# Optimization experiments

Measured on AMD Instinct MI355X. Metric: run time of the kernel, lower is better.

## Reference

```python
import jax, jax.numpy as jnp
import numpy as np

S, R, CM, CZ, H = 128, 256, 256, 128, 8
HD = CM // H
INF = 1e9
EPS = 1e-5


def _ln(x, g, b):
    mu = jnp.mean(x, axis=-1, keepdims=True)
    var = jnp.var(x, axis=-1, keepdims=True)
    return (x - mu) * jax.lax.rsqrt(var + EPS) * g + b


def setup_inputs() -> dict:
    key = jax.random.key(0)
    ks = jax.random.split(key, 12)
    d = {
        'm': jax.random.normal(ks[0], (S, R, CM), jnp.float32),
        'z': jax.random.normal(ks[1], (R, R, CZ), jnp.float32),
        'mask': jnp.ones((S, R), jnp.float32),
        'ln_m_g': jnp.ones((CM,), jnp.float32),
        'ln_m_b': jnp.zeros((CM,), jnp.float32),
        'ln_z_g': jnp.ones((CZ,), jnp.float32),
        'ln_z_b': jnp.zeros((CZ,), jnp.float32),
        'w_z': jax.random.normal(ks[2], (CZ, H), jnp.float32) * 0.02,
        'wq': jax.random.normal(ks[3], (CM, CM), jnp.float32) * (1.0 / np.sqrt(CM)),
        'wk': jax.random.normal(ks[4], (CM, CM), jnp.float32) * (1.0 / np.sqrt(CM)),
        'wv': jax.random.normal(ks[5], (CM, CM), jnp.float32) * (1.0 / np.sqrt(CM)),
        'wg': jnp.zeros((CM, CM), jnp.float32),
        'bg': jnp.ones((CM,), jnp.float32),
        'wo': jax.random.normal(ks[6], (CM, CM), jnp.float32) * (1.0 / np.sqrt(CM)),
        'bo': jnp.zeros((CM,), jnp.float32),
    }
    return d


def reference(m, z, mask, ln_m_g, ln_m_b, ln_z_g, ln_z_b, w_z, wq, wk, wv, wg, bg, wo, bo):
    # pair bias: LN(z) -> per-head bias [H, R, R], broadcast over seq rows
    z_ln = _ln(z, ln_z_g, ln_z_b)
    pair_bias = jnp.einsum('ijc,ch->hij', z_ln, w_z)          # [H, R, R]
    mask_bias = (INF * (mask - 1.0))[:, None, None, :]        # [S, 1, 1, R]

    m_ln = _ln(m, ln_m_g, ln_m_b)                             # [S, R, CM]
    q = (m_ln @ wq).reshape(S, R, H, HD)
    k = (m_ln @ wk).reshape(S, R, H, HD)
    v = (m_ln @ wv).reshape(S, R, H, HD)

    scale = 1.0 / np.sqrt(HD).astype(np.float32)
    logits = jnp.einsum('sihd,sjhd->shij', q * scale, k)       # [S, H, R, R]
    logits = logits + pair_bias[None] + mask_bias
    attn = jax.nn.softmax(logits, axis=-1)

    o = jnp.einsum('shij,sjhd->sihd', attn, v).reshape(S, R, CM)
    g = jax.nn.sigmoid(m_ln @ wg + bg)
    return (g * o) @ wo + bo
```

## Files before the change

### kernel.cpp

```cpp
#include <hip/hip_runtime.h>
#include <hip/hip_bf16.h>

typedef unsigned short u16;
typedef __bf16 bf16x8 __attribute__((ext_vector_type(8)));
typedef float f32x4 __attribute__((ext_vector_type(4)));
typedef float f32x16 __attribute__((ext_vector_type(16)));
typedef unsigned short u16x8 __attribute__((ext_vector_type(8)));
typedef unsigned short u16x4 __attribute__((ext_vector_type(4)));


__device__ __forceinline__ u16 f2bf(float f) {
  union { float f; unsigned u; } v; v.f = f;
  unsigned r = v.u;
  r += 0x7fffu + ((r >> 16) & 1u);
  return (u16)(r >> 16);
}
__device__ __forceinline__ float bf2f(u16 u) {
  union { unsigned u; float f; } v; v.u = ((unsigned)u) << 16;
  return v.f;
}

__global__ __launch_bounds__(256) void k_prep_w(
    const float* __restrict__ wq, const float* __restrict__ wk,
    const float* __restrict__ wv, const float* __restrict__ wg,
    const float* __restrict__ wo, u16* __restrict__ dst) {
  const int widx = blockIdx.x >> 4;
  const int tid = blockIdx.x & 15;
  const int ri = (tid >> 2) * 64;
  const int ci = (tid & 3) * 64;
  const float* src = (widx == 0) ? wq : (widx == 1) ? wk : (widx == 2) ? wv
                    : (widx == 3) ? wg : wo;
  __shared__ float lt[64][68];
  const int t = threadIdx.x;
  {
    const int r = t >> 2;
    #pragma unroll
    for (int i = 0; i < 4; ++i) {
      const int c = (t & 3) * 16 + i * 4;
      *(float4*)&lt[r][c] = *(const float4*)&src[(ri + r) * 256 + ci + c];
    }
  }
  __syncthreads();
  #pragma unroll
  for (int cc = 0; cc < 2; ++cc) {
    const int c = t + cc * 256;
    const int kb = c >> 8, cb = (c >> 6) & 3, lg = (c >> 4) & 3, lr = c & 15;
    u16x8 o;
    #pragma unroll
    for (int j = 0; j < 8; ++j) o[j] = f2bf(lt[kb * 32 + lg * 8 + j][cb * 16 + lr]);
    const size_t idx = (size_t)widx * 65536 + (size_t)((ci >> 4) + cb) * 4096
                     + (size_t)((ri >> 5) + kb) * 512 + (size_t)(lg * 16 + lr) * 8;
    *(u16x8*)&dst[idx] = o;
  }
}

__global__ __launch_bounds__(256) void k_pair_bias(
    const float* __restrict__ z, const float* __restrict__ zg,
    const float* __restrict__ zb, const float* __restrict__ wz,
    float* __restrict__ pbp) {
  const int t = threadIdx.x;
  const int lane = t & 63, wave = t >> 6;
  const int ql = lane & 15;
  const int p = blockIdx.x * 16 + wave * 4 + (lane >> 4);
  const float4 zv0 = *(const float4*)(z + (size_t)p * 128 + ql * 8);
  const float4 zv1 = *(const float4*)(z + (size_t)p * 128 + ql * 8 + 4);
  float s = zv0.x + zv0.y + zv0.z + zv0.w + zv1.x + zv1.y + zv1.z + zv1.w;
  float sq = zv0.x * zv0.x + zv0.y * zv0.y + zv0.z * zv0.z + zv0.w * zv0.w
           + zv1.x * zv1.x + zv1.y * zv1.y + zv1.z * zv1.z + zv1.w * zv1.w;
  #pragma unroll
  for (int o = 8; o > 0; o >>= 1) { s += __shfl_xor(s, o); sq += __shfl_xor(sq, o); }
  const float mu = s * 0.0078125f;
  const float var = sq * 0.0078125f - mu * mu;
  const float rs = rsqrtf(var + 1e-5f);
  const int c0 = ql * 8;
  float zn[8];
  zn[0] = (zv0.x - mu) * rs * zg[c0 + 0] + zb[c0 + 0];
  zn[1] = (zv0.y - mu) * rs * zg[c0 + 1] + zb[c0 + 1];
  zn[2] = (zv0.z - mu) * rs * zg[c0 + 2] + zb[c0 + 2];
  zn[3] = (zv0.w - mu) * rs * zg[c0 + 3] + zb[c0 + 3];
  zn[4] = (zv1.x - mu) * rs * zg[c0 + 4] + zb[c0 + 4];
  zn[5] = (zv1.y - mu) * rs * zg[c0 + 5] + zb[c0 + 5];
  zn[6] = (zv1.z - mu) * rs * zg[c0 + 6] + zb[c0 + 6];
  zn[7] = (zv1.w - mu) * rs * zg[c0 + 7] + zb[c0 + 7];
  float a[8] = {};
  #pragma unroll
  for (int i = 0; i < 8; ++i) {
    #pragma unroll
    for (int hh = 0; hh < 8; ++hh) a[hh] += zn[i] * wz[(c0 + i) * 8 + hh];
  }
  #pragma unroll
  for (int hh = 0; hh < 8; ++hh) {
    #pragma unroll
    for (int o = 8; o > 0; o >>= 1) a[hh] += __shfl_xor(a[hh], o);
  }
  if (ql == 0) {
    const int i = p >> 8, j = p & 255;
    const int strip = i >> 5, il = i & 31, jt = j >> 5, r = j & 31;
    const int gh = (r >> 2) & 1, qd = r >> 3, c4 = r & 3;
    const int off = (strip * 8 + jt) * 1024 + (gh * 32 + il) * 16 + qd * 4 + c4;
    #pragma unroll
    for (int hh = 0; hh < 8; ++hh) pbp[(size_t)hh * 65536 + off] = a[hh];
  }
}

__global__ __launch_bounds__(256) void k_ln_m(
    const float* __restrict__ m, const float* __restrict__ gam,
    const float* __restrict__ bet, u16* __restrict__ mln) {
  const int lane = threadIdx.x & 63;
  const size_t row = (size_t)blockIdx.x * 4 + (threadIdx.x >> 6);
  const float4 xv = *(const float4*)(m + row * 256 + lane * 4);
  float s = xv.x + xv.y + xv.z + xv.w;
  float sq = xv.x * xv.x + xv.y * xv.y + xv.z * xv.z + xv.w * xv.w;
  #pragma unroll
  for (int o = 32; o > 0; o >>= 1) { s += __shfl_xor(s, o); sq += __shfl_xor(sq, o); }
  const float mu = s * 0.00390625f;
  const float var = sq * 0.00390625f - mu * mu;
  const float rs = rsqrtf(var + 1e-5f);
  const int c = lane * 4;
  u16x4 o4;
  o4.x = f2bf((xv.x - mu) * rs * gam[c] + bet[c]);
  o4.y = f2bf((xv.y - mu) * rs * gam[c + 1] + bet[c + 1]);
  o4.z = f2bf((xv.z - mu) * rs * gam[c + 2] + bet[c + 2]);
  o4.w = f2bf((xv.w - mu) * rs * gam[c + 3] + bet[c + 3]);
  *(u16x4*)(mln + row * 256 + c) = o4;
}

__global__ __launch_bounds__(256, 2) void k_fused(
    const u16* __restrict__ mln, const u16* __restrict__ wtp,
    const float* __restrict__ bg, const float* __restrict__ pbp,
    const float* __restrict__ mask, u16* __restrict__ g,
    u16* __restrict__ go) {
  __shared__ u16 lA[32 * 256];
  __shared__ u16 lQ[256 * 32];
  __shared__ u16 lK[256 * 32];
  __shared__ u16 lVt[32][276];
  __shared__ float lMb[256];
  __shared__ float lL[4][32];
  const int bid = blockIdx.x;
  const int s = bid & 127, h = bid >> 7;
  const int t = threadIdx.x;
  const int lane = t & 63, wave = t >> 6;
  const int il = lane & 31, gh = lane >> 5;

  const u16* Wb = wtp + (size_t)wave * 65536 + (size_t)(2 * h + (il >> 4)) * 4096
                + gh * 128 + (il & 15) * 8;
  bf16x8 B[16];
  #pragma unroll
  for (int kc = 0; kc < 16; ++kc) B[kc] = *(const bf16x8*)&Wb[kc * 256];
  __builtin_amdgcn_sched_barrier(0);

  lMb[t] = 1e9f * (mask[s * 256 + t] - 1.0f);
  const float bgv = bg[h * 32 + il];
  const size_t mbase = (size_t)s * 65536;

  #pragma unroll 1
  for (int c = 0; c < 8; ++c) {
    #pragma unroll
    for (int i = 0; i < 4; ++i) {
      const int r = i * 8 + (t >> 5);
      const int cc = (t & 31) * 8;
      *(u16x8*)((char*)lA + ((r * 512 + cc * 2) ^ ((r & 7) << 4))) =
          *(const u16x8*)&mln[mbase + (size_t)(c * 32 + r) * 256 + cc];
    }
    __syncthreads();
    f32x16 acc = {};
    #pragma unroll
    for (int kc = 0; kc < 16; ++kc) {
      const bf16x8 af = *(const bf16x8*)((const char*)lA +
          ((il * 512 + (kc * 16 + gh * 8) * 2) ^ ((il & 7) << 4)));
      acc = __builtin_amdgcn_mfma_f32_32x32x16_bf16(af, B[kc], acc, 0, 0, 0);
    }
    if (wave == 0) {
      #pragma unroll
      for (int reg = 0; reg < 16; ++reg) {
        const int R = c * 32 + (reg & 3) + 8 * (reg >> 2) + 4 * gh;
        *(u16*)((char*)lQ + ((R * 64 + il * 2) ^ ((R & 7) << 4))) =
            f2bf(acc[reg] * 0.17677669529663687f);
      }
    } else if (wave == 1) {
      #pragma unroll
      for (int reg = 0; reg < 16; ++reg) {
        const int R = c * 32 + (reg & 3) + 8 * (reg >> 2) + 4 * gh;
        *(u16*)((char*)lK + ((R * 64 + il * 2) ^ ((R & 7) << 4))) = f2bf(acc[reg]);
      }
    } else if (wave == 2) {
      #pragma unroll
      for (int reg = 0; reg < 16; ++reg) {
        const int R = c * 32 + (reg & 3) + 8 * (reg >> 2) + 4 * gh;
        lVt[il][R] = f2bf(acc[reg]);
      }
    } else {
      #pragma unroll
      for (int reg = 0; reg < 16; ++reg) {
        const int R = c * 32 + (reg & 3) + 8 * (reg >> 2) + 4 * gh;
        const float x = acc[reg] + bgv;
        g[(size_t)(s * 256 + R) * 256 + h * 32 + il] =
            f2bf(1.0f / (1.0f + __expf(-x)));
      }
    }
    __syncthreads();
  }

  #pragma unroll 1
  for (int strip = 0; strip < 2; ++strip) {
    const int i0 = wave * 64 + strip * 32;
    bf16x8 qf[2];
    #pragma unroll
    for (int kk = 0; kk < 2; ++kk) {
      const int row = i0 + il;
      qf[kk] = *(const bf16x8*)((const char*)lQ +
          ((row * 64 + (kk * 16 + gh * 8) * 2) ^ ((row & 7) << 4)));
    }
    const float* pbt = pbp + ((size_t)h * 8 + (i0 >> 5)) * 8192 + lane * 16;

    f32x16 oacc0 = {}, oacc1 = {};
    float s0 = 0.f, s1 = 0.f, s2 = 0.f, s3 = 0.f;

    #pragma unroll 2
    for (int jt = 0; jt < 8; ++jt) {
      const float* pl = pbt + jt * 1024;
      f32x16 c;
      #pragma unroll
      for (int qd = 0; qd < 4; ++qd) {
        const f32x4 pbq = *(const f32x4*)&pl[qd * 4];
        const int jb = jt * 32 + qd * 8 + gh * 4;
        #pragma unroll
        for (int c4 = 0; c4 < 4; ++c4)
          c[qd * 4 + c4] = pbq[c4] + lMb[jb + c4] - 16.0f;
      }
      const int krow = jt * 32 + il;
      const bf16x8 kf0 = *(const bf16x8*)((const char*)lK +
          ((krow * 64 + (gh * 8) * 2) ^ ((krow & 7) << 4)));
      const bf16x8 kf1 = *(const bf16x8*)((const char*)lK +
          ((krow * 64 + (16 + gh * 8) * 2) ^ ((krow & 7) << 4)));
      c = __builtin_amdgcn_mfma_f32_32x32x16_bf16(kf0, qf[0], c, 0, 0, 0);
      c = __builtin_amdgcn_mfma_f32_32x32x16_bf16(kf1, qf[1], c, 0, 0, 0);
      union PK { __bf16 h[4]; uint2 u; } pk[4];
      #pragma unroll
      for (int qd = 0; qd < 4; ++qd) {
        const float p0 = __expf(c[qd * 4 + 0]);
        const float p1 = __expf(c[qd * 4 + 1]);
        const float p2 = __expf(c[qd * 4 + 2]);
        const float p3 = __expf(c[qd * 4 + 3]);
        s0 += p0; s1 += p1; s2 += p2; s3 += p3;
        pk[qd].h[0] = (__bf16)p0; pk[qd].h[1] = (__bf16)p1;
        pk[qd].h[2] = (__bf16)p2; pk[qd].h[3] = (__bf16)p3;
      }
      const uint2 sA = gh ? pk[0].u : pk[1].u;
      uint2 rA; rA.x = __shfl_xor(sA.x, 32); rA.y = __shfl_xor(sA.y, 32);
      const uint2 sB = gh ? pk[2].u : pk[3].u;
      uint2 rB; rB.x = __shfl_xor(sB.x, 32); rB.y = __shfl_xor(sB.y, 32);
      union FR { uint2 u2[2]; bf16x8 v; } fa0, fa1;
      fa0.u2[0] = gh ? rA : pk[0].u;
      fa0.u2[1] = gh ? pk[1].u : rA;
      fa1.u2[0] = gh ? rB : pk[2].u;
      fa1.u2[1] = gh ? pk[3].u : rB;
      const bf16x8 vf0 = *(const bf16x8*)&lVt[il][jt * 32 + gh * 8];
      const bf16x8 vf1 = *(const bf16x8*)&lVt[il][jt * 32 + 16 + gh * 8];
      oacc0 = __builtin_amdgcn_mfma_f32_32x32x16_bf16(fa0.v, vf0, oacc0, 0, 0, 0);
      oacc1 = __builtin_amdgcn_mfma_f32_32x32x16_bf16(fa1.v, vf1, oacc1, 0, 0, 0);
    }

    float lsum = (s0 + s1) + (s2 + s3);
    lsum += __shfl_xor(lsum, 32);
    if (lane < 32) lL[wave][il] = 1.0f / lsum;

    #pragma unroll
    for (int qd = 0; qd < 4; ++qd) {
      const f32x4 invq = *(const f32x4*)&lL[wave][qd * 8 + gh * 4];
      #pragma unroll
      for (int c4 = 0; c4 < 4; ++c4) {
        const int iloc = qd * 8 + gh * 4 + c4;
        const size_t row = (size_t)s * 256 + i0 + iloc;
        const int col = h * 32 + il;
        const float ov = (oacc0[qd * 4 + c4] + oacc1[qd * 4 + c4]) * invq[c4];
        go[row * 256 + col] = f2bf(bf2f(g[row * 256 + col]) * ov);
      }
    }
  }
}

__global__ __launch_bounds__(256, 4) void k_gemm_out(
    const u16* __restrict__ go, const u16* __restrict__ wop,
    const float* __restrict__ bo, float* __restrict__ out) {
  __shared__ u16 lA[32 * 256];
  const int t = threadIdx.x;
  const size_t row0 = (size_t)blockIdx.x * 32;
  const int lane = t & 63, wave = t >> 6;
  const u16* Wz = wop + (size_t)wave * 16384 + (size_t)lane * 8;
  u16x8 areg[4];
  #pragma unroll
  for (int i = 0; i < 4; ++i)
    areg[i] = *(const u16x8*)&go[(row0 + i * 8 + (t >> 5)) * 256 + (t & 31) * 8];
  bf16x8 B[4][4];
  #pragma unroll
  for (int kc = 0; kc < 4; ++kc) {
    #pragma unroll
    for (int nn = 0; nn < 4; ++nn)
      B[kc][nn] = *(const bf16x8*)&Wz[nn * 4096 + kc * 512];
  }
  __builtin_amdgcn_sched_barrier(0);
  #pragma unroll
  for (int i = 0; i < 4; ++i) {
    const int r = i * 8 + (t >> 5);
    const int c = (t & 31) * 8;
    *(u16x8*)((char*)lA + ((r * 512 + c * 2) ^ ((r & 7) << 4))) = areg[i];
  }
  __syncthreads();
  const int lrow = lane & 15, lg = lane >> 4;
  f32x4 acc[2][4] = {};
  #pragma unroll
  for (int kc = 0; kc < 4; ++kc) {
    bf16x8 af[2];
    #pragma unroll
    for (int mm = 0; mm < 2; ++mm) {
      const int row = mm * 16 + lrow;
      af[mm] = *(const bf16x8*)((const char*)lA +
          ((row * 512 + kc * 64 + lg * 16) ^ ((row & 7) << 4)));
    }
    #pragma unroll
    for (int mm = 0; mm < 2; ++mm) {
      #pragma unroll
      for (int nn = 0; nn < 4; ++nn)
        acc[mm][nn] = __builtin_amdgcn_mfma_f32_16x16x32_bf16(
            af[mm], B[kc][nn], acc[mm][nn], 0, 0, 0);
    }
  }
  #pragma unroll
  for (int kc = 0; kc < 4; ++kc) {
    #pragma unroll
    for (int nn = 0; nn < 4; ++nn)
      B[kc][nn] = *(const bf16x8*)&Wz[nn * 4096 + (kc + 4) * 512];
  }
  __builtin_amdgcn_sched_barrier(0);
  #pragma unroll
  for (int kc = 0; kc < 4; ++kc) {
    bf16x8 af[2];
    #pragma unroll
    for (int mm = 0; mm < 2; ++mm) {
      const int row = mm * 16 + lrow;
      af[mm] = *(const bf16x8*)((const char*)lA +
          ((row * 512 + (kc + 4) * 64 + lg * 16) ^ ((row & 7) << 4)));
    }
    #pragma unroll
    for (int mm = 0; mm < 2; ++mm) {
      #pragma unroll
      for (int nn = 0; nn < 4; ++nn)
        acc[mm][nn] = __builtin_amdgcn_mfma_f32_16x16x32_bf16(
            af[mm], B[kc][nn], acc[mm][nn], 0, 0, 0);
    }
  }
  const int wc = wave * 64, lg4 = lg * 4;
  #pragma unroll
  for (int mm = 0; mm < 2; ++mm) {
    #pragma unroll
    for (int nn = 0; nn < 4; ++nn) {
      const int col = wc + nn * 16 + lrow;
      #pragma unroll
      for (int jr = 0; jr < 4; ++jr) {
        const size_t row = row0 + mm * 16 + lg4 + jr;
        out[row * 256 + col] = acc[mm][nn][jr] + bo[col];
      }
    }
  }
}

extern "C" void kernel_launch(void* const* d_in, const int* in_sizes, int n_in,
                              void* d_out, int out_size, void* d_ws, size_t ws_size,
                              hipStream_t stream) {
  const float* m      = (const float*)d_in[0];
  const float* z      = (const float*)d_in[1];
  const float* mask   = (const float*)d_in[2];
  const float* ln_m_g = (const float*)d_in[3];
  const float* ln_m_b = (const float*)d_in[4];
  const float* ln_z_g = (const float*)d_in[5];
  const float* ln_z_b = (const float*)d_in[6];
  const float* w_z    = (const float*)d_in[7];
  const float* wq     = (const float*)d_in[8];
  const float* wk     = (const float*)d_in[9];
  const float* wv     = (const float*)d_in[10];
  const float* wg     = (const float*)d_in[11];
  const float* bg     = (const float*)d_in[12];
  const float* wo     = (const float*)d_in[13];
  const float* bo     = (const float*)d_in[14];
  float* out = (float*)d_out;

  char* w = (char*)d_ws;
  u16* wtp   = (u16*)w;   w += (size_t)5 * 65536 * 2;
  float* pbp = (float*)w; w += (size_t)8 * 65536 * 4;
  u16* mln   = (u16*)w;   w += (size_t)32768 * 256 * 2;
  u16* gow   = (u16*)w;   w += (size_t)32768 * 256 * 2;
  u16* gw    = (u16*)w;   w += (size_t)32768 * 256 * 2;

  k_prep_w   <<<80, 256, 0, stream>>>(wq, wk, wv, wg, wo, wtp);
  k_pair_bias<<<4096, 256, 0, stream>>>(z, ln_z_g, ln_z_b, w_z, pbp);
  k_ln_m     <<<8192, 256, 0, stream>>>(m, ln_m_g, ln_m_b, mln);
  k_fused    <<<1024, 256, 0, stream>>>(mln, wtp, bg, pbp, mask, gw, gow);
  k_gemm_out <<<1024, 256, 0, stream>>>(gow, wtp + (size_t)4 * 65536, bo, out);
}
```

Before: 122.9 us.

## Merge prep kernels, keep gate on-chip, prefetch A tiles, use exp2 softmax

```diff
diff --git a/kernel.cpp b/kernel.cpp
--- a/kernel.cpp
+++ b/kernel.cpp
@@ -8,128 +8,123 @@
 typedef unsigned short u16x8 __attribute__((ext_vector_type(8)));
 typedef unsigned short u16x4 __attribute__((ext_vector_type(4)));
 
-
-__device__ __forceinline__ u16 f2bf(float f) {
-  union { float f; unsigned u; } v; v.f = f;
-  unsigned r = v.u;
-  r += 0x7fffu + ((r >> 16) & 1u);
-  return (u16)(r >> 16);
+#define LOG2E 1.4426950408889634f
+
+__device__ __forceinline__ u16 f2b(float f) {
+  union { __bf16 b; u16 u; } v; v.b = (__bf16)f; return v.u;
 }
 __device__ __forceinline__ float bf2f(u16 u) {
   union { unsigned u; float f; } v; v.u = ((unsigned)u) << 16;
   return v.f;
 }
 
-__global__ __launch_bounds__(256) void k_prep_w(
+__global__ __launch_bounds__(256) void k_pre(
     const float* __restrict__ wq, const float* __restrict__ wk,
     const float* __restrict__ wv, const float* __restrict__ wg,
-    const float* __restrict__ wo, u16* __restrict__ dst) {
-  const int widx = blockIdx.x >> 4;
-  const int tid = blockIdx.x & 15;
-  const int ri = (tid >> 2) * 64;
-  const int ci = (tid & 3) * 64;
-  const float* src = (widx == 0) ? wq : (widx == 1) ? wk : (widx == 2) ? wv
-                    : (widx == 3) ? wg : wo;
-  __shared__ float lt[64][68];
-  const int t = threadIdx.x;
-  {
-    const int r = t >> 2;
-    #pragma unroll
-    for (int i = 0; i < 4; ++i) {
-      const int c = (t & 3) * 16 + i * 4;
-      *(float4*)&lt[r][c] = *(const float4*)&src[(ri + r) * 256 + ci + c];
-    }
-  }
-  __syncthreads();
-  #pragma unroll
-  for (int cc = 0; cc < 2; ++cc) {
-    const int c = t + cc * 256;
-    const int kb = c >> 8, cb = (c >> 6) & 3, lg = (c >> 4) & 3, lr = c & 15;
-    u16x8 o;
-    #pragma unroll
-    for (int j = 0; j < 8; ++j) o[j] = f2bf(lt[kb * 32 + lg * 8 + j][cb * 16 + lr]);
-    const size_t idx = (size_t)widx * 65536 + (size_t)((ci >> 4) + cb) * 4096
-                     + (size_t)((ri >> 5) + kb) * 512 + (size_t)(lg * 16 + lr) * 8;
-    *(u16x8*)&dst[idx] = o;
-  }
-}
-
-__global__ __launch_bounds__(256) void k_pair_bias(
+    const float* __restrict__ wo, u16* __restrict__ wtp,
     const float* __restrict__ z, const float* __restrict__ zg,
     const float* __restrict__ zb, const float* __restrict__ wz,
-    float* __restrict__ pbp) {
-  const int t = threadIdx.x;
-  const int lane = t & 63, wave = t >> 6;
-  const int ql = lane & 15;
-  const int p = blockIdx.x * 16 + wave * 4 + (lane >> 4);
-  const float4 zv0 = *(const float4*)(z + (size_t)p * 128 + ql * 8);
-  const float4 zv1 = *(const float4*)(z + (size_t)p * 128 + ql * 8 + 4);
-  float s = zv0.x + zv0.y + zv0.z + zv0.w + zv1.x + zv1.y + zv1.z + zv1.w;
-  float sq = zv0.x * zv0.x + zv0.y * zv0.y + zv0.z * zv0.z + zv0.w * zv0.w
-           + zv1.x * zv1.x + zv1.y * zv1.y + zv1.z * zv1.z + zv1.w * zv1.w;
-  #pragma unroll
-  for (int o = 8; o > 0; o >>= 1) { s += __shfl_xor(s, o); sq += __shfl_xor(sq, o); }
-  const float mu = s * 0.0078125f;
-  const float var = sq * 0.0078125f - mu * mu;
-  const float rs = rsqrtf(var + 1e-5f);
-  const int c0 = ql * 8;
-  float zn[8];
-  zn[0] = (zv0.x - mu) * rs * zg[c0 + 0] + zb[c0 + 0];
-  zn[1] = (zv0.y - mu) * rs * zg[c0 + 1] + zb[c0 + 1];
-  zn[2] = (zv0.z - mu) * rs * zg[c0 + 2] + zb[c0 + 2];
-  zn[3] = (zv0.w - mu) * rs * zg[c0 + 3] + zb[c0 + 3];
-  zn[4] = (zv1.x - mu) * rs * zg[c0 + 4] + zb[c0 + 4];
-  zn[5] = (zv1.y - mu) * rs * zg[c0 + 5] + zb[c0 + 5];
-  zn[6] = (zv1.z - mu) * rs * zg[c0 + 6] + zb[c0 + 6];
-  zn[7] = (zv1.w - mu) * rs * zg[c0 + 7] + zb[c0 + 7];
-  float a[8] = {};
-  #pragma unroll
-  for (int i = 0; i < 8; ++i) {
-    #pragma unroll
-    for (int hh = 0; hh < 8; ++hh) a[hh] += zn[i] * wz[(c0 + i) * 8 + hh];
-  }
-  #pragma unroll
-  for (int hh = 0; hh < 8; ++hh) {
-    #pragma unroll
-    for (int o = 8; o > 0; o >>= 1) a[hh] += __shfl_xor(a[hh], o);
-  }
-  if (ql == 0) {
-    const int i = p >> 8, j = p & 255;
-    const int strip = i >> 5, il = i & 31, jt = j >> 5, r = j & 31;
-    const int gh = (r >> 2) & 1, qd = r >> 3, c4 = r & 3;
-    const int off = (strip * 8 + jt) * 1024 + (gh * 32 + il) * 16 + qd * 4 + c4;
-    #pragma unroll
-    for (int hh = 0; hh < 8; ++hh) pbp[(size_t)hh * 65536 + off] = a[hh];
-  }
-}
-
-__global__ __launch_bounds__(256) void k_ln_m(
+    float* __restrict__ pbp,
     const float* __restrict__ m, const float* __restrict__ gam,
     const float* __restrict__ bet, u16* __restrict__ mln) {
-  const int lane = threadIdx.x & 63;
-  const size_t row = (size_t)blockIdx.x * 4 + (threadIdx.x >> 6);
-  const float4 xv = *(const float4*)(m + row * 256 + lane * 4);
-  float s = xv.x + xv.y + xv.z + xv.w;
-  float sq = xv.x * xv.x + xv.y * xv.y + xv.z * xv.z + xv.w * xv.w;
-  #pragma unroll
-  for (int o = 32; o > 0; o >>= 1) { s += __shfl_xor(s, o); sq += __shfl_xor(sq, o); }
-  const float mu = s * 0.00390625f;
-  const float var = sq * 0.00390625f - mu * mu;
-  const float rs = rsqrtf(var + 1e-5f);
-  const int c = lane * 4;
-  u16x4 o4;
-  o4.x = f2bf((xv.x - mu) * rs * gam[c] + bet[c]);
-  o4.y = f2bf((xv.y - mu) * rs * gam[c + 1] + bet[c + 1]);
-  o4.z = f2bf((xv.z - mu) * rs * gam[c + 2] + bet[c + 2]);
-  o4.w = f2bf((xv.w - mu) * rs * gam[c + 3] + bet[c + 3]);
-  *(u16x4*)(mln + row * 256 + c) = o4;
+  __shared__ float lt[64][68];
+  const int b = blockIdx.x;
+  const int t = threadIdx.x;
+  if (b < 80) {
+    const int widx = b >> 4;
+    const int tid = b & 15;
+    const int ri = (tid >> 2) * 64, ci = (tid & 3) * 64;
+    const float* src = (widx == 0) ? wq : (widx == 1) ? wk : (widx == 2) ? wv
+                      : (widx == 3) ? wg : wo;
+    {
+      const int r = t >> 2;
+      #pragma unroll
+      for (int i = 0; i < 4; ++i) {
+        const int c = (t & 3) * 16 + i * 4;
+        *(float4*)&lt[r][c] = *(const float4*)&src[(ri + r) * 256 + ci + c];
+      }
+    }
+    __syncthreads();
+    #pragma unroll
+    for (int cc = 0; cc < 2; ++cc) {
+      const int c = t + cc * 256;
+      const int kb = c >> 8, cb = (c >> 6) & 3, lg = (c >> 4) & 3, lr = c & 15;
+      u16x8 o;
+      #pragma unroll
+      for (int j = 0; j < 8; ++j) o[j] = f2b(lt[kb * 32 + lg * 8 + j][cb * 16 + lr]);
+      const size_t idx = (size_t)widx * 65536 + (size_t)((ci >> 4) + cb) * 4096
+                       + (size_t)((ri >> 5) + kb) * 512 + (size_t)(lg * 16 + lr) * 8;
+      *(u16x8*)&wtp[idx] = o;
+    }
+  } else if (b < 4176) {
+    const int lane = t & 63, wave = t >> 6;
+    const int ql = lane & 15;
+    const int p = (b - 80) * 16 + wave * 4 + (lane >> 4);
+    const float4 zv0 = *(const float4*)(z + (size_t)p * 128 + ql * 8);
+    const float4 zv1 = *(const float4*)(z + (size_t)p * 128 + ql * 8 + 4);
+    float s = zv0.x + zv0.y + zv0.z + zv0.w + zv1.x + zv1.y + zv1.z + zv1.w;
+    float sq = zv0.x * zv0.x + zv0.y * zv0.y + zv0.z * zv0.z + zv0.w * zv0.w
+             + zv1.x * zv1.x + zv1.y * zv1.y + zv1.z * zv1.z + zv1.w * zv1.w;
+    #pragma unroll
+    for (int o = 8; o > 0; o >>= 1) { s += __shfl_xor(s, o); sq += __shfl_xor(sq, o); }
+    const float mu = s * 0.0078125f;
+    const float var = sq * 0.0078125f - mu * mu;
+    const float rs = rsqrtf(var + 1e-5f);
+    const int c0 = ql * 8;
+    float zn[8];
+    zn[0] = (zv0.x - mu) * rs * zg[c0 + 0] + zb[c0 + 0];
+    zn[1] = (zv0.y - mu) * rs * zg[c0 + 1] + zb[c0 + 1];
+    zn[2] = (zv0.z - mu) * rs * zg[c0 + 2] + zb[c0 + 2];
+    zn[3] = (zv0.w - mu) * rs * zg[c0 + 3] + zb[c0 + 3];
+    zn[4] = (zv1.x - mu) * rs * zg[c0 + 4] + zb[c0 + 4];
+    zn[5] = (zv1.y - mu) * rs * zg[c0 + 5] + zb[c0 + 5];
+    zn[6] = (zv1.z - mu) * rs * zg[c0 + 6] + zb[c0 + 6];
+    zn[7] = (zv1.w - mu) * rs * zg[c0 + 7] + zb[c0 + 7];
+    float a[8] = {};
+    #pragma unroll
+    for (int i = 0; i < 8; ++i) {
+      #pragma unroll
+      for (int hh = 0; hh < 8; ++hh) a[hh] += zn[i] * wz[(c0 + i) * 8 + hh];
+    }
+    #pragma unroll
+    for (int hh = 0; hh < 8; ++hh) {
+      #pragma unroll
+      for (int o = 8; o > 0; o >>= 1) a[hh] += __shfl_xor(a[hh], o);
+    }
+    if (ql == 0) {
+      const int i = p >> 8, j = p & 255;
+      const int strip = i >> 5, il = i & 31, jt = j >> 5, r = j & 31;
+      const int gh = (r >> 2) & 1, qd = r >> 3, c4 = r & 3;
+      const int off = (strip * 8 + jt) * 1024 + (gh * 32 + il) * 16 + qd * 4 + c4;
+      #pragma unroll
+      for (int hh = 0; hh < 8; ++hh)
+        pbp[(size_t)hh * 65536 + off] = a[hh] * LOG2E;
+    }
+  } else {
+    const int lane = t & 63;
+    const size_t row = (size_t)(b - 4176) * 4 + (t >> 6);
+    const float4 xv = *(const float4*)(m + row * 256 + lane * 4);
+    float s = xv.x + xv.y + xv.z + xv.w;
+    float sq = xv.x * xv.x + xv.y * xv.y + xv.z * xv.z + xv.w * xv.w;
+    #pragma unroll
+    for (int o = 32; o > 0; o >>= 1) { s += __shfl_xor(s, o); sq += __shfl_xor(sq, o); }
+    const float mu = s * 0.00390625f;
+    const float var = sq * 0.00390625f - mu * mu;
+    const float rs = rsqrtf(var + 1e-5f);
+    const int c = lane * 4;
+    u16x4 o4;
+    o4.x = f2b((xv.x - mu) * rs * gam[c] + bet[c]);
+    o4.y = f2b((xv.y - mu) * rs * gam[c + 1] + bet[c + 1]);
+    o4.z = f2b((xv.z - mu) * rs * gam[c + 2] + bet[c + 2]);
+    o4.w = f2b((xv.w - mu) * rs * gam[c + 3] + bet[c + 3]);
+    *(u16x4*)(mln + row * 256 + c) = o4;
+  }
 }
 
 __global__ __launch_bounds__(256, 2) void k_fused(
     const u16* __restrict__ mln, const u16* __restrict__ wtp,
     const float* __restrict__ bg, const float* __restrict__ pbp,
-    const float* __restrict__ mask, u16* __restrict__ g,
-    u16* __restrict__ go) {
+    const float* __restrict__ mask, u16* __restrict__ go) {
   __shared__ u16 lA[32 * 256];
   __shared__ u16 lQ[256 * 32];
   __shared__ u16 lK[256 * 32];
@@ -149,57 +144,87 @@
   for (int kc = 0; kc < 16; ++kc) B[kc] = *(const bf16x8*)&Wb[kc * 256];
   __builtin_amdgcn_sched_barrier(0);
 
-  lMb[t] = 1e9f * (mask[s * 256 + t] - 1.0f);
+  lMb[t] = (LOG2E * 1e9f) * (mask[s * 256 + t] - 1.0f) - 24.0f;
   const float bgv = bg[h * 32 + il];
   const size_t mbase = (size_t)s * 65536;
 
-  #pragma unroll 1
+  u16x8 areg[4];
+  #pragma unroll
+  for (int i = 0; i < 4; ++i)
+    areg[i] = *(const u16x8*)&mln[mbase + (size_t)(i * 8 + (t >> 5)) * 256 + (t & 31) * 8];
+  unsigned gpk[64];
+
+  #pragma unroll
   for (int c = 0; c < 8; ++c) {
     #pragma unroll
     for (int i = 0; i < 4; ++i) {
       const int r = i * 8 + (t >> 5);
-      const int cc = (t & 31) * 8;
-      *(u16x8*)((char*)lA + ((r * 512 + cc * 2) ^ ((r & 7) << 4))) =
-          *(const u16x8*)&mln[mbase + (size_t)(c * 32 + r) * 256 + cc];
+      *(u16x8*)((char*)lA + ((r * 512 + (t & 31) * 16) ^ ((r & 7) << 4))) = areg[i];
     }
     __syncthreads();
-    f32x16 acc = {};
-    #pragma unroll
-    for (int kc = 0; kc < 16; ++kc) {
-      const bf16x8 af = *(const bf16x8*)((const char*)lA +
+    if (c < 7) {
+      #pragma unroll
+      for (int i = 0; i < 4; ++i)
+        areg[i] = *(const u16x8*)&mln[mbase +
+            (size_t)((c + 1) * 32 + i * 8 + (t >> 5)) * 256 + (t & 31) * 8];
+      __builtin_amdgcn_sched_barrier(0);
+    }
+    f32x16 a0 = {}, a1 = {};
+    #pragma unroll
+    for (int kc = 0; kc < 16; kc += 2) {
+      const bf16x8 af0 = *(const bf16x8*)((const char*)lA +
           ((il * 512 + (kc * 16 + gh * 8) * 2) ^ ((il & 7) << 4)));
-      acc = __builtin_amdgcn_mfma_f32_32x32x16_bf16(af, B[kc], acc, 0, 0, 0);
-    }
+      const bf16x8 af1 = *(const bf16x8*)((const char*)lA +
+          ((il * 512 + ((kc + 1) * 16 + gh * 8) * 2) ^ ((il & 7) << 4)));
+      a0 = __builtin_amdgcn_mfma_f32_32x32x16_bf16(af0, B[kc], a0, 0, 0, 0);
+      a1 = __builtin_amdgcn_mfma_f32_32x32x16_bf16(af1, B[kc + 1], a1, 0, 0, 0);
+    }
+    const f32x16 acc = a0 + a1;
     if (wave == 0) {
       #pragma unroll
       for (int reg = 0; reg < 16; ++reg) {
         const int R = c * 32 + (reg & 3) + 8 * (reg >> 2) + 4 * gh;
         *(u16*)((char*)lQ + ((R * 64 + il * 2) ^ ((R & 7) << 4))) =
-            f2bf(acc[reg] * 0.17677669529663687f);
+            f2b(acc[reg] * (0.17677669529663687f * LOG2E));
       }
     } else if (wave == 1) {
       #pragma unroll
       for (int reg = 0; reg < 16; ++reg) {
         const int R = c * 32 + (reg & 3) + 8 * (reg >> 2) + 4 * gh;
-        *(u16*)((char*)lK + ((R * 64 + il * 2) ^ ((R & 7) << 4))) = f2bf(acc[reg]);
+        *(u16*)((char*)lK + ((R * 64 + il * 2) ^ ((R & 7) << 4))) = f2b(acc[reg]);
       }
     } else if (wave == 2) {
       #pragma unroll
       for (int reg = 0; reg < 16; ++reg) {
         const int R = c * 32 + (reg & 3) + 8 * (reg >> 2) + 4 * gh;
-        lVt[il][R] = f2bf(acc[reg]);
+        lVt[il][R] = f2b(acc[reg]);
       }
     } else {
       #pragma unroll
-      for (int reg = 0; reg < 16; ++reg) {
-        const int R = c * 32 + (reg & 3) + 8 * (reg >> 2) + 4 * gh;
-        const float x = acc[reg] + bgv;
-        g[(size_t)(s * 256 + R) * 256 + h * 32 + il] =
-            f2bf(1.0f / (1.0f + __expf(-x)));
+      for (int r4 = 0; r4 < 8; ++r4) {
+        const float x0 = acc[2 * r4] + bgv;
+        const float x1 = acc[2 * r4 + 1] + bgv;
+        const u16 u0 = f2b(1.0f / (1.0f + __expf(-x0)));
+        const u16 u1 = f2b(1.0f / (1.0f + __expf(-x1)));
+        gpk[c * 8 + r4] = (unsigned)u0 | ((unsigned)u1 << 16);
       }
     }
     __syncthreads();
   }
+
+  if (wave == 3) {
+    #pragma unroll
+    for (int c = 0; c < 8; ++c) {
+      #pragma unroll
+      for (int r4 = 0; r4 < 8; ++r4) {
+        const int R0 = c * 32 + ((2 * r4) & 3) + 8 * (r4 >> 1) + 4 * gh;
+        const unsigned p = gpk[c * 8 + r4];
+        lA[R0 * 32 + il] = (u16)p;
+        lA[(R0 + 1) * 32 + il] = (u16)(p >> 16);
+      }
+    }
+  }
+  __syncthreads();
 
   #pragma unroll 1
   for (int strip = 0; strip < 2; ++strip) {
@@ -226,7 +251,7 @@
         const int jb = jt * 32 + qd * 8 + gh * 4;
         #pragma unroll
         for (int c4 = 0; c4 < 4; ++c4)
-          c[qd * 4 + c4] = pbq[c4] + lMb[jb + c4] - 16.0f;
+          c[qd * 4 + c4] = pbq[c4] + lMb[jb + c4];
       }
       const int krow = jt * 32 + il;
       const bf16x8 kf0 = *(const bf16x8*)((const char*)lK +
@@ -238,10 +263,10 @@
       union PK { __bf16 h[4]; uint2 u; } pk[4];
       #pragma unroll
       for (int qd = 0; qd < 4; ++qd) {
-        const float p0 = __expf(c[qd * 4 + 0]);
-        const float p1 = __expf(c[qd * 4 + 1]);
-        const float p2 = __expf(c[qd * 4 + 2]);
-        const float p3 = __expf(c[qd * 4 + 3]);
+        const float p0 = exp2f(c[qd * 4 + 0]);
+        const float p1 = exp2f(c[qd * 4 + 1]);
+        const float p2 = exp2f(c[qd * 4 + 2]);
+        const float p3 = exp2f(c[qd * 4 + 3]);
         s0 += p0; s1 += p1; s2 += p2; s3 += p3;
         pk[qd].h[0] = (__bf16)p0; pk[qd].h[1] = (__bf16)p1;
         pk[qd].h[2] = (__bf16)p2; pk[qd].h[3] = (__bf16)p3;
@@ -274,7 +299,8 @@
         const size_t row = (size_t)s * 256 + i0 + iloc;
         const int col = h * 32 + il;
         const float ov = (oacc0[qd * 4 + c4] + oacc1[qd * 4 + c4]) * invq[c4];
-        go[row * 256 + col] = f2bf(bf2f(g[row * 256 + col]) * ov);
+        const float gv = bf2f(lA[(i0 + iloc) * 32 + il]);
+        go[row * 256 + col] = f2b(gv * ov);
       }
     }
   }
@@ -390,11 +416,10 @@
   float* pbp = (float*)w; w += (size_t)8 * 65536 * 4;
   u16* mln   = (u16*)w;   w += (size_t)32768 * 256 * 2;
   u16* gow   = (u16*)w;   w += (size_t)32768 * 256 * 2;
-  u16* gw    = (u16*)w;   w += (size_t)32768 * 256 * 2;
-
-  k_prep_w   <<<80, 256, 0, stream>>>(wq, wk, wv, wg, wo, wtp);
-  k_pair_bias<<<4096, 256, 0, stream>>>(z, ln_z_g, ln_z_b, w_z, pbp);
-  k_ln_m     <<<8192, 256, 0, stream>>>(m, ln_m_g, ln_m_b, mln);
-  k_fused    <<<1024, 256, 0, stream>>>(mln, wtp, bg, pbp, mask, gw, gow);
+
+  k_pre      <<<12368, 256, 0, stream>>>(wq, wk, wv, wg, wo, wtp,
+                                         z, ln_z_g, ln_z_b, w_z, pbp,
+                                         m, ln_m_g, ln_m_b, mln);
+  k_fused    <<<1024, 256, 0, stream>>>(mln, wtp, bg, pbp, mask, gow);
   k_gemm_out <<<1024, 256, 0, stream>>>(gow, wtp + (size_t)4 * 65536, bo, out);
 }
```

New measurement: 114.4 us. -6.9%, faster.
